# Kernel optimization log

Measured on AMD Instinct MI355X. Metric: run time of the kernel, lower is better.

## Reference

```python
import jax, jax.numpy as jnp
from jax import lax
import numpy as np

ALPHA = 0.5   # weight of shape vs temporal component
GAMMA = 0.01  # soft-min temperature
BIG = 1e10    # finite stand-in for +inf borders (safe gradients)


def _softmin3(a, b, c, gamma):
    # -gamma * logsumexp(-x/gamma) over the three candidates
    z = jnp.stack([a, b, c], axis=0)
    return -gamma * jax.nn.logsumexp(-z / gamma, axis=0)


def _softdtw(D, gamma):
    """Soft-DTW value per problem. D: (B, N, N) cost matrix -> (B,).
    Classic DP: R[i,j] = D[i-1,j-1] + softmin(R[i-1,j-1], R[i-1,j], R[i,j-1])."""
    B, N, _ = D.shape
    # R row 0: R[0,0]=0, R[0,j>=1]=inf
    row0 = jnp.concatenate(
        [jnp.zeros((B, 1), D.dtype), jnp.full((B, N), BIG, D.dtype)], axis=1)
    left_init = jnp.full((B,), BIG, D.dtype)  # R[i,0] = inf for i>=1

    def row_step(R_prev, d_row):  # d_row: (B, N) = D[:, i-1, :]
        # per column j: diag = R_prev[j-1], up = R_prev[j], left = carry
        xs = (d_row.T, R_prev[:, :-1].T, R_prev[:, 1:].T)  # each (N, B)

        def col_step(r_left, x):
            d, r_diag, r_up = x
            r = d + _softmin3(r_diag, r_up, r_left, gamma)
            return r, r

        _, vals = lax.scan(col_step, left_init, xs)  # (N, B)
        R_row = jnp.concatenate([left_init[:, None], vals.T], axis=1)  # (B, N+1)
        return R_row, None

    R_last, _ = lax.scan(row_step, row0, jnp.transpose(D, (1, 0, 2)))
    return R_last[:, -1]  # R[N, N]


def _dilate(inp, tgt):
    B, C, N = inp.shape
    t = tgt.reshape(B * C, N)
    p = inp.reshape(B * C, N)
    # pairwise squared distances between 1-d points: D[k,i,j] = (t_i - p_j)^2
    D = (t[:, :, None] - p[:, None, :]) ** 2  # (B*C, N, N)

    # shape loss = soft-DTW value, averaged over channels
    sdtw = _softdtw(D, GAMMA)  # (B*C,)
    loss_shape = sdtw.reshape(B, C).mean(axis=1)  # (B,)

    # soft alignment path = gradient of soft-DTW w.r.t. the cost matrix
    E = jax.grad(lambda d: _softdtw(d, GAMMA).sum())(D)  # (B*C, N, N)

    # Omega[i,j] = (i - j)^2 temporal penalty
    idx = jnp.arange(1, N + 1, dtype=D.dtype)
    Omega = (idx[:, None] - idx[None, :]) ** 2  # (N, N)

    lt = jnp.sum(E * Omega, axis=(1, 2)) / (N * N)  # (B*C,)
    loss_temporal = lt.reshape(B, C).mean(axis=1)  # (B,)

    loss = (ALPHA * loss_shape + (1.0 - ALPHA) * loss_temporal).mean()
    return loss, loss_shape, loss_temporal


def setup_inputs() -> dict:
    key = jax.random.key(0)
    k1, k2 = jax.random.split(key)
    B, C, N = 64, 8, 160
    return {
        "input": jax.random.normal(k1, (B, C, N), jnp.float32),
        "target": jax.random.normal(k2, (B, C, N), jnp.float32),
    }


def reference(input, target):
    return _dilate(input, target)
```

## Files before the change

kernel.cpp:

```cpp
#include <hip/hip_runtime.h>
#include <math.h>


#define NN     160
#define BC_TOT 512
#define B_SZ   64
#define C_SZ   8
#define BIGC2  1e12f
#define SC2    12.01122405f
#define GLN2   0.0069314718056f

__device__ __forceinline__ float fexp2(float x) {
#if __has_builtin(__builtin_amdgcn_exp2f)
    return __builtin_amdgcn_exp2f(x);
#else
    return exp2f(x);
#endif
}
__device__ __forceinline__ float flog2(float x) {
#if __has_builtin(__builtin_amdgcn_logf)
    return __builtin_amdgcn_logf(x);
#else
    return log2f(x);
#endif
}
__device__ __forceinline__ float frcp(float x) {
#if __has_builtin(__builtin_amdgcn_rcpf)
    return __builtin_amdgcn_rcpf(x);
#else
    return 1.0f / x;
#endif
}
__device__ __forceinline__ float dpp_up1_inj(float old, float x) {
    int oi = __builtin_bit_cast(int, old);
    int xi = __builtin_bit_cast(int, x);
    return __builtin_bit_cast(float,
        __builtin_amdgcn_update_dpp(oi, xi, 0x138, 0xF, 0xF, false));
}

#define STEP(PV0) do {                                                        \
                   \
    const float mn0 = fminf(b0, fminf(a0, r0));                               \
    const float ed0 = fexp2(mn0 - b0);           \
    const float ev0 = fexp2(mn0 - a0);                                        \
    const float eh0 = fexp2(mn0 - r0);                                        \
    const float ss0 = ed0 + ev0 + eh0;                                        \
    const float rs0 = frcp(ss0);                                              \
    const float dt0 = trS0 - (PV0);                                           \
    const float n0  = __builtin_fmaf(dt0, dt0, mn0) - flog2(ss0);             \
    const float nm0 = __builtin_fmaf(ed0, bd0,                                \
                      __builtin_fmaf(ev0, ad0, eh0 * g0));                    \
    const float om0 = dj0 * dj0;                                              \
    const float nd0 = __builtin_fmaf(nm0, rs0, om0);                          \
                                \
    const float mn1 = fminf(b1, fminf(a1, r1));                               \
    const float ed1 = fexp2(mn1 - b1);                                        \
    const float ev1 = fexp2(mn1 - a1);                                        \
    const float eh1 = fexp2(mn1 - r1);                                        \
    const float ss1 = ed1 + ev1 + eh1;                                        \
    const float rs1 = frcp(ss1);                                              \
    const float dt1 = trS1 - pva;                                             \
    const float n1  = __builtin_fmaf(dt1, dt1, mn1) - flog2(ss1);             \
    const float nm1 = __builtin_fmaf(ed1, bd1,                                \
                      __builtin_fmaf(ev1, ad1, eh1 * g1));                    \
    const float dj1 = dj0 - 2.0f;                                             \
    const float nd1 = __builtin_fmaf(nm1, rs1, dj1 * dj1);                    \
                                \
    const float mn2 = fminf(b2, fminf(a2, r2));                               \
    const float ed2 = fexp2(mn2 - b2);                                        \
    const float ev2 = fexp2(mn2 - a2);                                        \
    const float eh2 = fexp2(mn2 - r2);                                        \
    const float ss2 = ed2 + ev2 + eh2;                                        \
    const float rs2 = frcp(ss2);                                              \
    const float dt2 = trS2 - pvb;                                             \
    const float n2  = __builtin_fmaf(dt2, dt2, mn2) - flog2(ss2);             \
    const float nm2 = __builtin_fmaf(ed2, bd2,                                \
                      __builtin_fmaf(ev2, ad2, eh2 * g2));                    \
    const float dj2 = dj0 - 4.0f;                                             \
    const float nd2 = __builtin_fmaf(nm2, rs2, dj2 * dj2);                    \
                   \
    b2 = a2;  bd2 = ad2;  a2 = n1;  ad2 = nd1;                                \
    b1 = a1;  bd1 = ad1;  a1 = n0;  ad1 = nd0;                                \
    b0 = a0;  bd0 = ad0;                                                      \
    a0  = dpp_up1_inj(BIGC2, n2);              \
    ad0 = dpp_up1_inj(0.0f,  nd2);            \
    r0 = n0; r1 = n1; r2 = n2;                                                \
    g0 = nd0; g1 = nd1; g2 = nd2;                                             \
    pvb = pva; pva = (PV0);                                                   \
    dj0 += 1.0f;                                                              \
} while (0)

__global__ __launch_bounds__(64, 1)
void dtw_fwd_kernel(const float* __restrict__ input,
                    const float* __restrict__ target,
                    float* __restrict__ sdtw,
                    float* __restrict__ wlt)
{
    const int k    = blockIdx.x;
    const int lane = threadIdx.x;

    __shared__ __align__(16) float Pp[512];

    const float* tg = target + (size_t)k * NN;
    const float* pg = input  + (size_t)k * NN;
    #pragma unroll
    for (int x0 = 0; x0 < 512; x0 += 64) {
        const int x = x0 + lane;
        const int v = x - 192;
        Pp[x] = ((unsigned)v < (unsigned)NN) ? pg[v] * SC2 : 0.0f;
    }
    const int r3 = 3 * lane;
    const float trS0 = (r3 + 0 < NN) ? tg[r3 + 0] * SC2 : 0.0f;
    const float trS1 = (r3 + 1 < NN) ? tg[r3 + 1] * SC2 : 0.0f;
    const float trS2 = (r3 + 2 < NN) ? tg[r3 + 2] * SC2 : 0.0f;
    __asm__ __volatile__("" ::: "memory");
    __builtin_amdgcn_s_waitcnt(0xC07F);
    __asm__ __volatile__("" ::: "memory");

    float r0 = BIGC2, r1 = BIGC2, r2 = BIGC2;
    float g0 = 0.0f,  g1 = 0.0f,  g2 = 0.0f;
    float a0 = BIGC2, a1 = BIGC2, a2 = BIGC2;
    float ad0 = 0.0f, ad1 = 0.0f, ad2 = 0.0f;
    float b0 = (lane == 0) ? 0.0f : BIGC2;
    float b1 = BIGC2, b2 = BIGC2;
    float bd0 = 0.0f, bd1 = 0.0f, bd2 = 0.0f;

    float pva = 0.0f, pvb = 0.0f;
    float dj0 = (float)(-6 * lane);

    const int pb = 192 - r3;
    float pf0 = Pp[pb + 0], pf1 = Pp[pb + 1], pf2 = Pp[pb + 2], pf3 = Pp[pb + 3];

    for (int tb = 0; tb < 79; ++tb) {
        const int tn = 4 * tb + 4;
        const float q0 = Pp[pb + tn + 0];
        const float q1 = Pp[pb + tn + 1];
        const float q2 = Pp[pb + tn + 2];
        const float q3 = Pp[pb + tn + 3];
        STEP(pf0); STEP(pf1); STEP(pf2); STEP(pf3);
        pf0 = q0; pf1 = q1; pf2 = q2; pf3 = q3;
    }
    STEP(pf0); STEP(pf1); STEP(pf2);

    if (lane == 53) {
        sdtw[k] = r0 * GLN2;
        wlt[k]  = g0 * (1.0f / (NN * NN));
    }
}

__global__ __launch_bounds__(64)
void finalize_kernel(const float* __restrict__ sdtw,
                     const float* __restrict__ wlt,
                     float* __restrict__ out)
{
    const int b = threadIdx.x;
    float ls = 0.0f, lt = 0.0f;
    #pragma unroll
    for (int c = 0; c < C_SZ; ++c) {
        ls += sdtw[b * C_SZ + c];
        lt += wlt[b * C_SZ + c];
    }
    ls *= (1.0f / C_SZ);
    lt *= (1.0f / C_SZ);
    out[1 + b]        = ls;
    out[1 + B_SZ + b] = lt;
    float v = 0.5f * ls + 0.5f * lt;
    #pragma unroll
    for (int o = 32; o > 0; o >>= 1) v += __shfl_down(v, o);
    if (b == 0) out[0] = v * (1.0f / B_SZ);
}

extern "C" void kernel_launch(void* const* d_in, const int* in_sizes, int n_in,
                              void* d_out, int out_size, void* d_ws, size_t ws_size,
                              hipStream_t stream) {
    const float* input  = (const float*)d_in[0];
    const float* target = (const float*)d_in[1];
    float* out = (float*)d_out;

    float* sdtw = (float*)d_ws;
    float* wlt  = sdtw + BC_TOT;

    dtw_fwd_kernel<<<BC_TOT, 64, 0, stream>>>(input, target, sdtw, wlt);
    finalize_kernel<<<1, 64, 0, stream>>>(sdtw, wlt, out);
}
```

Baseline: 101.4 us.

## Split DTW wavefront across two waves with LDS ring handoff

Splits each 160-row soft-DTW wavefront across two 64-lane waves, each handling 80 rows at 2 rows per lane instead of 3. The first wave's boundary lane publishes its last row's values into an LDS ring buffer. The second wave spin-waits on a NaN sentinel before consuming them. This shortens the per-step serial work per lane and doubles the threads per block. In exchange it adds LDS traffic, volatile polling, and a pipeline delay of 80 rows (320 steps total instead of 239).

```diff
diff --git a/kernel.cpp b/kernel.cpp
--- a/kernel.cpp
+++ b/kernel.cpp
@@ -9,6 +9,8 @@
 #define BIGC2  1e12f
 #define SC2    12.01122405f
 #define GLN2   0.0069314718056f
+#define SENT_I 0x7FC00000
+#define RSLOTS 336
 
 __device__ __forceinline__ float fexp2(float x) {
 #if __has_builtin(__builtin_amdgcn_exp2f)
@@ -38,113 +40,113 @@
         __builtin_amdgcn_update_dpp(oi, xi, 0x138, 0xF, 0xF, false));
 }
 
-#define STEP(PV0) do {                                                        \
-                   \
+#define STEP(PV0, T_) do {                                                    \
+    float rvx = BIGC2, rvy = 0.0f;                                            \
+    const volatile float* rp_ = (const volatile float*)&ring[(T_)];           \
+    if (cons) { rvx = rp_[0]; rvy = rp_[1]; }    \
     const float mn0 = fminf(b0, fminf(a0, r0));                               \
+    const float mn1 = fminf(b1, fminf(a1, r1));                               \
     const float ed0 = fexp2(mn0 - b0);           \
     const float ev0 = fexp2(mn0 - a0);                                        \
     const float eh0 = fexp2(mn0 - r0);                                        \
-    const float ss0 = ed0 + ev0 + eh0;                                        \
-    const float rs0 = frcp(ss0);                                              \
-    const float dt0 = trS0 - (PV0);                                           \
-    const float n0  = __builtin_fmaf(dt0, dt0, mn0) - flog2(ss0);             \
-    const float nm0 = __builtin_fmaf(ed0, bd0,                                \
-                      __builtin_fmaf(ev0, ad0, eh0 * g0));                    \
-    const float om0 = dj0 * dj0;                                              \
-    const float nd0 = __builtin_fmaf(nm0, rs0, om0);                          \
-                                \
-    const float mn1 = fminf(b1, fminf(a1, r1));                               \
     const float ed1 = fexp2(mn1 - b1);                                        \
     const float ev1 = fexp2(mn1 - a1);                                        \
     const float eh1 = fexp2(mn1 - r1);                                        \
-    const float ss1 = ed1 + ev1 + eh1;                                        \
+    const float ss0 = (ed0 + ev0) + eh0;                            \
+    const float ss1 = (ed1 + ev1) + eh1;                                      \
+    const float rs0 = frcp(ss0);                                              \
     const float rs1 = frcp(ss1);                                              \
+    const float dt0 = trS0 - (PV0);                                           \
     const float dt1 = trS1 - pva;                                             \
-    const float n1  = __builtin_fmaf(dt1, dt1, mn1) - flog2(ss1);             \
+    const float n0 = __builtin_fmaf(dt0, dt0, mn0) - flog2(ss0);              \
+    const float n1 = __builtin_fmaf(dt1, dt1, mn1) - flog2(ss1);              \
+    const float nm0 = __builtin_fmaf(ed0, bd0,                                \
+                      __builtin_fmaf(ev0, ad0, eh0 * g0));                    \
     const float nm1 = __builtin_fmaf(ed1, bd1,                                \
                       __builtin_fmaf(ev1, ad1, eh1 * g1));                    \
     const float dj1 = dj0 - 2.0f;                                             \
+    const float nd0 = __builtin_fmaf(nm0, rs0, dj0 * dj0);                    \
     const float nd1 = __builtin_fmaf(nm1, rs1, dj1 * dj1);                    \
-                                \
-    const float mn2 = fminf(b2, fminf(a2, r2));                               \
-    const float ed2 = fexp2(mn2 - b2);                                        \
-    const float ev2 = fexp2(mn2 - a2);                                        \
-    const float eh2 = fexp2(mn2 - r2);                                        \
-    const float ss2 = ed2 + ev2 + eh2;                                        \
-    const float rs2 = frcp(ss2);                                              \
-    const float dt2 = trS2 - pvb;                                             \
-    const float n2  = __builtin_fmaf(dt2, dt2, mn2) - flog2(ss2);             \
-    const float nm2 = __builtin_fmaf(ed2, bd2,                                \
-                      __builtin_fmaf(ev2, ad2, eh2 * g2));                    \
-    const float dj2 = dj0 - 4.0f;                                             \
-    const float nd2 = __builtin_fmaf(nm2, rs2, dj2 * dj2);                    \
-                   \
-    b2 = a2;  bd2 = ad2;  a2 = n1;  ad2 = nd1;                                \
-    b1 = a1;  bd1 = ad1;  a1 = n0;  ad1 = nd0;                                \
-    b0 = a0;  bd0 = ad0;                                                      \
-    a0  = dpp_up1_inj(BIGC2, n2);              \
-    ad0 = dpp_up1_inj(0.0f,  nd2);            \
-    r0 = n0; r1 = n1; r2 = n2;                                                \
-    g0 = nd0; g1 = nd1; g2 = nd2;                                             \
-    pvb = pva; pva = (PV0);                                                   \
-    dj0 += 1.0f;                                                              \
+    if (pub) {                \
+        volatile float* wp_ = (volatile float*)&ring[(T_) + 1];               \
+        wp_[1] = nd1;                                                         \
+        wp_[0] = n1;                                                          \
+    }                                                                         \
+    if (cons) {           \
+        while (__builtin_amdgcn_readfirstlane(                                \
+                   __builtin_bit_cast(int, rvx)) == (int)SENT_I) {            \
+            rvx = rp_[0]; rvy = rp_[1];                                       \
+        }                                                                     \
+    }                                                                         \
+    b1 = a1; bd1 = ad1; a1 = n0; ad1 = nd0;                                   \
+    b0 = a0; bd0 = ad0;                                                       \
+    a0  = dpp_up1_inj(rvx, n1);             \
+    ad0 = dpp_up1_inj(rvy, nd1);                                              \
+    r0 = n0; r1 = n1; g0 = nd0; g1 = nd1;                                     \
+    pva = (PV0); dj0 += 1.0f;                                                 \
 } while (0)
 
-__global__ __launch_bounds__(64, 1)
+__global__ __launch_bounds__(128, 1)
 void dtw_fwd_kernel(const float* __restrict__ input,
                     const float* __restrict__ target,
                     float* __restrict__ sdtw,
                     float* __restrict__ wlt)
 {
     const int k    = blockIdx.x;
-    const int lane = threadIdx.x;
+    const int tid  = threadIdx.x;
+    const int wv   = tid >> 6;
+    const int lane = tid & 63;
 
-    __shared__ __align__(16) float Pp[512];
+    __shared__ __align__(16) float  Pp[544];
+    __shared__ __align__(8)  float2 ring[RSLOTS];
 
     const float* tg = target + (size_t)k * NN;
     const float* pg = input  + (size_t)k * NN;
-    #pragma unroll
-    for (int x0 = 0; x0 < 512; x0 += 64) {
-        const int x = x0 + lane;
+    for (int x = tid; x < 544; x += 128) {
         const int v = x - 192;
         Pp[x] = ((unsigned)v < (unsigned)NN) ? pg[v] * SC2 : 0.0f;
     }
-    const int r3 = 3 * lane;
-    const float trS0 = (r3 + 0 < NN) ? tg[r3 + 0] * SC2 : 0.0f;
-    const float trS1 = (r3 + 1 < NN) ? tg[r3 + 1] * SC2 : 0.0f;
-    const float trS2 = (r3 + 2 < NN) ? tg[r3 + 2] * SC2 : 0.0f;
-    __asm__ __volatile__("" ::: "memory");
-    __builtin_amdgcn_s_waitcnt(0xC07F);
-    __asm__ __volatile__("" ::: "memory");
+    for (int x = tid; x < RSLOTS; x += 128) {
+        float2 z;
+        z.x = (x == 0) ? BIGC2 : __builtin_bit_cast(float, (int)SENT_I);
+        z.y = 0.0f;
+        ring[x] = z;
+    }
+    const int  rowb = 80 * wv + 2 * lane;
+    const bool act  = (lane < 40);
+    const float trS0 = act ? tg[rowb]     * SC2 : 0.0f;
+    const float trS1 = act ? tg[rowb + 1] * SC2 : 0.0f;
+    __syncthreads();
 
-    float r0 = BIGC2, r1 = BIGC2, r2 = BIGC2;
-    float g0 = 0.0f,  g1 = 0.0f,  g2 = 0.0f;
-    float a0 = BIGC2, a1 = BIGC2, a2 = BIGC2;
-    float ad0 = 0.0f, ad1 = 0.0f, ad2 = 0.0f;
-    float b0 = (lane == 0) ? 0.0f : BIGC2;
-    float b1 = BIGC2, b2 = BIGC2;
-    float bd0 = 0.0f, bd1 = 0.0f, bd2 = 0.0f;
+    const bool pub  = (wv == 0) && (lane == 39);
+    const bool cons = (wv == 1);
 
-    float pva = 0.0f, pvb = 0.0f;
-    float dj0 = (float)(-6 * lane);
+    float r0 = BIGC2, r1 = BIGC2, g0 = 0.0f, g1 = 0.0f;
+    float a0 = BIGC2, a1 = BIGC2, ad0 = 0.0f, ad1 = 0.0f;
+    float b0 = (wv == 0 && lane == 0) ? 0.0f : BIGC2;
+    float b1 = BIGC2, bd0 = 0.0f, bd1 = 0.0f;
+    float pva = 0.0f;
+    float dj0 = (wv == 0) ? (float)(-4 * lane) : (float)(-4 * lane - 161);
+    int pb = (wv == 0) ? (192 - 2 * lane) : (111 - 2 * lane);
+    if (pb < 0) pb = 0;
 
-    const int pb = 192 - r3;
     float pf0 = Pp[pb + 0], pf1 = Pp[pb + 1], pf2 = Pp[pb + 2], pf3 = Pp[pb + 3];
 
     for (int tb = 0; tb < 79; ++tb) {
-        const int tn = 4 * tb + 4;
-        const float q0 = Pp[pb + tn + 0];
-        const float q1 = Pp[pb + tn + 1];
-        const float q2 = Pp[pb + tn + 2];
-        const float q3 = Pp[pb + tn + 3];
-        STEP(pf0); STEP(pf1); STEP(pf2); STEP(pf3);
+        const int t4 = 4 * tb;
+        const float q0 = Pp[pb + t4 + 4];
+        const float q1 = Pp[pb + t4 + 5];
+        const float q2 = Pp[pb + t4 + 6];
+        const float q3 = Pp[pb + t4 + 7];
+        STEP(pf0, t4 + 0); STEP(pf1, t4 + 1);
+        STEP(pf2, t4 + 2); STEP(pf3, t4 + 3);
         pf0 = q0; pf1 = q1; pf2 = q2; pf3 = q3;
     }
-    STEP(pf0); STEP(pf1); STEP(pf2);
+    STEP(pf0, 316); STEP(pf1, 317); STEP(pf2, 318); STEP(pf3, 319);
 
-    if (lane == 53) {
-        sdtw[k] = r0 * GLN2;
-        wlt[k]  = g0 * (1.0f / (NN * NN));
+    if (wv == 1 && lane == 39) {
+        sdtw[k] = r1 * GLN2;
+        wlt[k]  = g1 * (1.0f / (NN * NN));
     }
 }
 
@@ -180,6 +182,6 @@
     float* sdtw = (float*)d_ws;
     float* wlt  = sdtw + BC_TOT;
 
-    dtw_fwd_kernel<<<BC_TOT, 64, 0, stream>>>(input, target, sdtw, wlt);
+    dtw_fwd_kernel<<<BC_TOT, 128, 0, stream>>>(input, target, sdtw, wlt);
     finalize_kernel<<<1, 64, 0, stream>>>(sdtw, wlt, out);
 }
```

Result: slower. 146.8 us (+44.8%).
